# Performance work log

Hardware: AMD Instinct MI355X
Metric: run time of the kernel (lower is better)

## Reference

```python
import jax, jax.numpy as jnp
import numpy as np

MODEL_DIM = 1024
NUM_HEADS = 8
B, L = 16, 2048


def setup_inputs() -> dict:
    key = jax.random.key(0)
    ks = jax.random.split(key, 12)
    s = 1.0 / np.sqrt(MODEL_DIM)
    d = MODEL_DIM
    return {
        "query": jax.random.normal(ks[0], (B, L, d), jnp.float32),
        "key_": jax.random.normal(ks[1], (B, L, d), jnp.float32),
        "value": jax.random.normal(ks[2], (B, L, d), jnp.float32),
        "Wq": jax.random.uniform(ks[3], (d, d), jnp.float32, -s, s),
        "bq": jax.random.uniform(ks[4], (d,), jnp.float32, -s, s),
        "Wk": jax.random.uniform(ks[5], (d, d), jnp.float32, -s, s),
        "bk": jax.random.uniform(ks[6], (d,), jnp.float32, -s, s),
        "Wv": jax.random.uniform(ks[7], (d, d), jnp.float32, -s, s),
        "bv": jax.random.uniform(ks[8], (d,), jnp.float32, -s, s),
        "Wo": jax.random.uniform(ks[9], (d, d), jnp.float32, -s, s),
        "bo": jax.random.uniform(ks[10], (d,), jnp.float32, -s, s),
    }


def reference(query, key_, value, Wq, bq, Wk, bk, Wv, bv, Wo, bo):
    # NOTE: the original module does NOT split heads; attention is over the
    # full model_dim per batch row. num_heads only enters via the scale.
    residual = query
    q = jnp.einsum("bld,de->ble", query, Wq) + bq
    k = jnp.einsum("bld,de->ble", key_, Wk) + bk
    v = jnp.einsum("bld,de->ble", value, Wv) + bv
    scale = (MODEL_DIM // NUM_HEADS) ** (-0.5)
    attn = jnp.einsum("bqd,bkd->bqk", q, k) * scale  # [B, L, L]
    attn = jax.nn.softmax(attn, axis=-1)
    ctx = jnp.einsum("bqk,bkd->bqd", attn, v)
    out = jnp.einsum("bld,de->ble", ctx, Wo) + bo  # dropout=0.0 -> identity
    return residual + out
```

## Files before the change

### kernel.cpp

```cpp
#include <hip/hip_runtime.h>
#include <cstdint>

#define B_ 16
#define L_ 2048
#define D_ 1024
#define BLROWS (B_ * L_)
#define QK_SCALE 0.08838834764831845f

typedef unsigned short u16;
typedef __attribute__((ext_vector_type(8))) __bf16 bf16x8;
typedef __attribute__((ext_vector_type(4))) float f32x4;
typedef __attribute__((ext_vector_type(4))) unsigned int u32x4;
typedef __attribute__((ext_vector_type(4))) u16 u16x4;

__device__ __forceinline__ u16 f2bf(float f) {
  unsigned u = __builtin_bit_cast(unsigned, f);
  u += 0x7fffu + ((u >> 16) & 1u);
  return (u16)(u >> 16);
}
__device__ __forceinline__ float bf2f(unsigned hu) {
  return __builtin_bit_cast(float, hu << 16);
}

__device__ __forceinline__ void gll16(const void* g, void* l) {
  auto gp = reinterpret_cast<const __attribute__((address_space(1))) unsigned int*>(
      reinterpret_cast<uintptr_t>(g));
  auto lp = reinterpret_cast<__attribute__((address_space(3))) unsigned int*>(
      reinterpret_cast<uintptr_t>(l));
  __builtin_amdgcn_global_load_lds(gp, lp, 16, 0, 0);
}

typedef __attribute__((ext_vector_type(4))) float fv4;
__global__ void convert_bf16(const fv4* __restrict__ in, u16x4* __restrict__ out, int n4) {
  int i = blockIdx.x * blockDim.x + threadIdx.x;
  const int stride = gridDim.x * blockDim.x;
  for (; i < n4; i += stride) {
    fv4 v = in[i];
    u16x4 o;
    o.x = f2bf(v.x); o.y = f2bf(v.y); o.z = f2bf(v.z); o.w = f2bf(v.w);
    out[i] = o;
  }
}

__global__ void transpose_convert_1k(const float* __restrict__ W, u16* __restrict__ WT) {
  __shared__ float tile[32][33];
  const int bx = blockIdx.x * 32;
  const int by = blockIdx.y * 32;
  const int tx = threadIdx.x & 31;
  const int ty = threadIdx.x >> 5;
#pragma unroll
  for (int j = 0; j < 4; ++j) {
    const int r = ty + j * 8;
    tile[r][tx] = W[(size_t)(by + r) * 1024 + bx + tx];
  }
  __syncthreads();
#pragma unroll
  for (int j = 0; j < 4; ++j) {
    const int r = ty + j * 8;
    WT[(size_t)(bx + r) * 1024 + by + tx] = f2bf(tile[tx][r]);
  }
}

__global__ void softmax_rows(u16* __restrict__ S) {
  const size_t row = blockIdx.x;
  u32x4* p = (u32x4*)(S + row * 2048);
  const int t = threadIdx.x;
  u32x4 v = p[t];
  unsigned vv[4] = {v.x, v.y, v.z, v.w};
  float x[8];
#pragma unroll
  for (int i = 0; i < 4; ++i) {
    x[2 * i]     = bf2f(vv[i] & 0xffffu);
    x[2 * i + 1] = bf2f(vv[i] >> 16);
  }
  float m = x[0];
#pragma unroll
  for (int i = 1; i < 8; ++i) m = fmaxf(m, x[i]);
#pragma unroll
  for (int off = 32; off > 0; off >>= 1) m = fmaxf(m, __shfl_xor(m, off));
  __shared__ float red[4];
  const int w = t >> 6, l = t & 63;
  if (l == 0) red[w] = m;
  __syncthreads();
  m = fmaxf(fmaxf(red[0], red[1]), fmaxf(red[2], red[3]));
  float e[8], s = 0.f;
#pragma unroll
  for (int i = 0; i < 8; ++i) { e[i] = __expf(x[i] - m); s += e[i]; }
#pragma unroll
  for (int off = 32; off > 0; off >>= 1) s += __shfl_xor(s, off);
  __syncthreads();
  if (l == 0) red[w] = s;
  __syncthreads();
  s = red[0] + red[1] + red[2] + red[3];
  const float inv = 1.0f / s;
  unsigned oo[4];
#pragma unroll
  for (int i = 0; i < 4; ++i) {
    oo[i] = (unsigned)f2bf(e[2 * i] * inv) | ((unsigned)f2bf(e[2 * i + 1] * inv) << 16);
  }
  u32x4 o; o.x = oo[0]; o.y = oo[1]; o.z = oo[2]; o.w = oo[3];
  p[t] = o;
}


#define MFMA16(QM, QN, BF)                                                    \
  _Pragma("unroll") for (int mf = 0; mf < 4; ++mf)                            \
  _Pragma("unroll") for (int nf = 0; nf < 2; ++nf)                            \
  _Pragma("unroll") for (int kk = 0; kk < 2; ++kk)                            \
      acc[(QM)*4 + mf][(QN)*2 + nf] = __builtin_amdgcn_mfma_f32_16x16x32_bf16( \
          af[mf][kk], BF[nf][kk], acc[(QM)*4 + mf][(QN)*2 + nf], 0, 0, 0);

template <int OUT_BF16, int BIAS_MODE, int RESID>
__global__ __launch_bounds__(512) void gemm8(
    const u16* __restrict__ A, const u16* __restrict__ Bm, void* __restrict__ Cv,
    const float* __restrict__ bias, const float* __restrict__ resid,
    int N, int K, float scale, long long sA, long long sB, long long sC,
    int gm, int gn) {
  __shared__ alignas(16) u16 lds[2][4][128 * 64];

  const int nwg = gridDim.x;
  const int wg = blockIdx.x;
  const int q = nwg >> 3, rr = nwg & 7;
  const int xcd = wg & 7, idx = wg >> 3;
  const int wgid = (xcd < rr ? xcd * (q + 1) : rr * (q + 1) + (xcd - rr) * q) + idx;
  const int z = wgid / (gm * gn);
  const int rem = wgid - z * gm * gn;
  const int my = rem / gn;
  const int nx = rem - my * gn;
  const int m0 = my * 256, n0 = nx * 256;

  A  += (long long)z * sA;
  Bm += (long long)z * sB;

  const int t = threadIdx.x;
  const int w = t >> 6;
  const int l = t & 63;
  const int wm = w >> 2;
  const int wn = w & 3;
  const int lr = l & 15;
  const int lk = l >> 4;

  const int r  = t >> 3;
  const int sl = (t & 7) ^ (r & 7);
  const u16* pa00 = A  + (long long)(m0 +   0 + r) * K + sl * 8;
  const u16* pa01 = A  + (long long)(m0 +  64 + r) * K + sl * 8;
  const u16* pa10 = A  + (long long)(m0 + 128 + r) * K + sl * 8;
  const u16* pa11 = A  + (long long)(m0 + 192 + r) * K + sl * 8;
  const u16* pb00 = Bm + (long long)(n0 +   0 + r) * K + sl * 8;
  const u16* pb01 = Bm + (long long)(n0 +  64 + r) * K + sl * 8;
  const u16* pb10 = Bm + (long long)(n0 + 128 + r) * K + sl * 8;
  const u16* pb11 = Bm + (long long)(n0 + 192 + r) * K + sl * 8;
  const int wo = w * 512;

#define STAGE_TILE_A(LB, KT)                         \
  gll16(pa00 + (KT)*64, (LB) + 0 * 8192 +        wo); \
  gll16(pa01 + (KT)*64, (LB) + 0 * 8192 + 4096 + wo); \
  gll16(pa10 + (KT)*64, (LB) + 1 * 8192 +        wo); \
  gll16(pa11 + (KT)*64, (LB) + 1 * 8192 + 4096 + wo);
#define STAGE_TILE_B(LB, KT)                         \
  gll16(pb00 + (KT)*64, (LB) + 2 * 8192 +        wo); \
  gll16(pb01 + (KT)*64, (LB) + 2 * 8192 + 4096 + wo); \
  gll16(pb10 + (KT)*64, (LB) + 3 * 8192 +        wo); \
  gll16(pb11 + (KT)*64, (LB) + 3 * 8192 + 4096 + wo);

  f32x4 acc[8][4];
#pragma unroll
  for (int i = 0; i < 8; ++i)
#pragma unroll
    for (int j = 0; j < 4; ++j) acc[i][j] = f32x4{0.f, 0.f, 0.f, 0.f};

  const int cs0 = ((0 + lk) ^ (lr & 7)) * 8;
  const int cs1 = ((4 + lk) ^ (lr & 7)) * 8;
  const u16* LA = &lds[0][wm][0];
  const u16* LB_ = &lds[0][2 + (wn >> 1)][0];
  const int brow = (wn & 1) * 64 + lr;

  {
    u16* Lb = &lds[0][0][0];
    STAGE_TILE_A(Lb, 0)
    STAGE_TILE_B(Lb, 0)
  }
  asm volatile("s_waitcnt vmcnt(0)" ::: "memory");
  __builtin_amdgcn_s_barrier();
  __builtin_amdgcn_sched_barrier(0);

  const int NT = K >> 6;
  for (int kt = 0; kt < NT; ++kt) {
    const int br = kt & 1, bs = br ^ 1;
    const bool pf = (kt + 1 < NT);
    const u16* Ra = LA + br * 32768;
    const u16* Rb = LB_ + br * 32768;
    u16* Lb = &lds[bs][0][0];

    bf16x8 af[4][2], bf0[2][2], bf1[2][2];

    if (pf) { STAGE_TILE_A(Lb, kt + 1) }
#pragma unroll
    for (int mf = 0; mf < 4; ++mf) {
      const int row = mf * 16 + lr;
      af[mf][0] = __builtin_bit_cast(bf16x8, *(const u32x4*)&Ra[row * 64 + cs0]);
      af[mf][1] = __builtin_bit_cast(bf16x8, *(const u32x4*)&Ra[row * 64 + cs1]);
    }
#pragma unroll
    for (int nf = 0; nf < 2; ++nf) {
      const int row = brow + nf * 16;
      bf0[nf][0] = __builtin_bit_cast(bf16x8, *(const u32x4*)&Rb[row * 64 + cs0]);
      bf0[nf][1] = __builtin_bit_cast(bf16x8, *(const u32x4*)&Rb[row * 64 + cs1]);
    }
    __builtin_amdgcn_s_barrier();
    __builtin_amdgcn_s_setprio(1);
    MFMA16(0, 0, bf0)
    __builtin_amdgcn_s_setprio(0);
    __builtin_amdgcn_s_barrier();

    if (pf) { STAGE_TILE_B(Lb, kt + 1) }
#pragma unroll
    for (int nf = 0; nf < 2; ++nf) {
      const int row = brow + 32 + nf * 16;
      bf1[nf][0] = __builtin_bit_cast(bf16x8, *(const u32x4*)&Rb[row * 64 + cs0]);
      bf1[nf][1] = __builtin_bit_cast(bf16x8, *(const u32x4*)&Rb[row * 64 + cs1]);
    }
    __builtin_amdgcn_s_barrier();
    __builtin_amdgcn_s_setprio(1);
    MFMA16(0, 1, bf1)
    __builtin_amdgcn_s_setprio(0);
    __builtin_amdgcn_s_barrier();

#pragma unroll
    for (int mf = 0; mf < 4; ++mf) {
      const int row = 64 + mf * 16 + lr;
      af[mf][0] = __builtin_bit_cast(bf16x8, *(const u32x4*)&Ra[row * 64 + cs0]);
      af[mf][1] = __builtin_bit_cast(bf16x8, *(const u32x4*)&Ra[row * 64 + cs1]);
    }
    __builtin_amdgcn_s_barrier();
    __builtin_amdgcn_s_setprio(1);
    MFMA16(1, 1, bf1)
    __builtin_amdgcn_s_setprio(0);
    __builtin_amdgcn_s_barrier();

    __builtin_amdgcn_s_setprio(1);
    MFMA16(1, 0, bf0)
    __builtin_amdgcn_s_setprio(0);

    if (pf) { asm volatile("s_waitcnt vmcnt(0)" ::: "memory"); }
    __builtin_amdgcn_s_barrier();
    __builtin_amdgcn_sched_barrier(0);
  }

  const int crow0 = m0 + wm * 128;
  const int ccol0 = n0 + wn * 64;
#pragma unroll
  for (int mi = 0; mi < 8; ++mi) {
#pragma unroll
    for (int i = 0; i < 4; ++i) {
      const int grow = crow0 + (mi >> 2) * 64 + (mi & 3) * 16 + lk * 4 + i;
#pragma unroll
      for (int nj = 0; nj < 4; ++nj) {
        const int gcol = ccol0 + (nj >> 1) * 32 + (nj & 1) * 16 + lr;
        float v = acc[mi][nj][i] * scale;
        if (BIAS_MODE == 1) v += bias[gcol];
        if (BIAS_MODE == 2) v += bias[grow];
        if (RESID) v += resid[(long long)grow * N + gcol];
        const long long cidx = (long long)z * sC + (long long)grow * N + gcol;
        if (OUT_BF16) ((u16*)Cv)[cidx] = f2bf(v);
        else          ((float*)Cv)[cidx] = v;
      }
    }
  }
}

extern "C" void kernel_launch(void* const* d_in, const int* in_sizes, int n_in,
                              void* d_out, int out_size, void* d_ws, size_t ws_size,
                              hipStream_t stream) {
  const float* query = (const float*)d_in[0];
  const float* key_  = (const float*)d_in[1];
  const float* value = (const float*)d_in[2];
  const float* Wq = (const float*)d_in[3];
  const float* bq = (const float*)d_in[4];
  const float* Wk = (const float*)d_in[5];
  const float* bk = (const float*)d_in[6];
  const float* Wv = (const float*)d_in[7];
  const float* bv = (const float*)d_in[8];
  const float* Wo = (const float*)d_in[9];
  const float* bo = (const float*)d_in[10];
  float* out = (float*)d_out;

  char* ws = (char*)d_ws;
  u16* xq  = (u16*)(ws + 0);
  u16* xk  = (u16*)(ws + 67108864);
  u16* xv  = (u16*)(ws + 134217728);
  u16* wqt = (u16*)(ws + 201326592);
  u16* wkt = (u16*)(ws + 203423744);
  u16* wvt = (u16*)(ws + 205520896);
  u16* wot = (u16*)(ws + 207618048);
  u16* qb  = (u16*)(ws + 209715200);
  u16* kb  = (u16*)(ws + 276824064);
  u16* vt  = (u16*)(ws + 343932928);
  u16* sp  = (u16*)(ws + 0);
  u16* ctx = (u16*)(ws + 134217728);

  const dim3 blk(256);
  const dim3 blk8(512);
  const int n4 = BLROWS * D_ / 4;

  convert_bf16<<<2048, blk, 0, stream>>>((const fv4*)query, (u16x4*)xq, n4);
  convert_bf16<<<2048, blk, 0, stream>>>((const fv4*)key_,  (u16x4*)xk, n4);
  convert_bf16<<<2048, blk, 0, stream>>>((const fv4*)value, (u16x4*)xv, n4);
  transpose_convert_1k<<<dim3(32, 32), blk, 0, stream>>>(Wq, wqt);
  transpose_convert_1k<<<dim3(32, 32), blk, 0, stream>>>(Wk, wkt);
  transpose_convert_1k<<<dim3(32, 32), blk, 0, stream>>>(Wv, wvt);
  transpose_convert_1k<<<dim3(32, 32), blk, 0, stream>>>(Wo, wot);

  gemm8<1, 1, 0><<<dim3(512), blk8, 0, stream>>>(
      xq, wqt, qb, bq, nullptr, D_, D_, 1.0f, 0, 0, 0, 128, 4);
  gemm8<1, 1, 0><<<dim3(512), blk8, 0, stream>>>(
      xk, wkt, kb, bk, nullptr, D_, D_, 1.0f, 0, 0, 0, 128, 4);
  gemm8<1, 2, 0><<<dim3(512), blk8, 0, stream>>>(
      wvt, xv, vt, bv, nullptr, L_, D_, 1.0f,
      0, (long long)L_ * D_, (long long)D_ * L_, 4, 8);
  gemm8<1, 0, 0><<<dim3(1024), blk8, 0, stream>>>(
      qb, kb, sp, nullptr, nullptr, L_, D_, QK_SCALE,
      (long long)L_ * D_, (long long)L_ * D_, (long long)L_ * L_, 8, 8);
  softmax_rows<<<BLROWS, blk, 0, stream>>>(sp);
  gemm8<1, 0, 0><<<dim3(512), blk8, 0, stream>>>(
      sp, vt, ctx, nullptr, nullptr, D_, L_, 1.0f,
      (long long)L_ * L_, (long long)D_ * L_, (long long)L_ * D_, 8, 4);
  gemm8<0, 1, 1><<<dim3(512), blk8, 0, stream>>>(
      ctx, wot, out, bo, query, D_, D_, 1.0f, 0, 0, 0, 128, 4);

  (void)in_sizes; (void)n_in; (void)out_size; (void)ws_size;
}
```

Before: 1.070 ms.

## Restructure GEMM mainloop to 4-stage K=32 LDS pipeline with prefetch depth three

Replaces the double-buffered K=64 tile loop with a four-buffer ring of K=32 slices, keeping three slices of global-to-LDS loads in flight by using partial vmcnt waits instead of draining all loads each iteration. The LDS layout and XOR swizzle change to 32-element rows, and each wave's output fragments are remapped to contiguous 16-row/16-column blocks. The aim is to hide global memory latency behind MFMA work. In exchange, each iteration does half the math between barriers, so barrier overhead per unit of work roughly doubles. The epilogue index mapping changes to match the new fragment layout.

```diff
diff --git a/kernel.cpp b/kernel.cpp
--- a/kernel.cpp
+++ b/kernel.cpp
@@ -103,20 +103,13 @@
 }
 
 
-#define MFMA16(QM, QN, BF)                                                    \
-  _Pragma("unroll") for (int mf = 0; mf < 4; ++mf)                            \
-  _Pragma("unroll") for (int nf = 0; nf < 2; ++nf)                            \
-  _Pragma("unroll") for (int kk = 0; kk < 2; ++kk)                            \
-      acc[(QM)*4 + mf][(QN)*2 + nf] = __builtin_amdgcn_mfma_f32_16x16x32_bf16( \
-          af[mf][kk], BF[nf][kk], acc[(QM)*4 + mf][(QN)*2 + nf], 0, 0, 0);
-
 template <int OUT_BF16, int BIAS_MODE, int RESID>
 __global__ __launch_bounds__(512) void gemm8(
     const u16* __restrict__ A, const u16* __restrict__ Bm, void* __restrict__ Cv,
     const float* __restrict__ bias, const float* __restrict__ resid,
     int N, int K, float scale, long long sA, long long sB, long long sC,
     int gm, int gn) {
-  __shared__ alignas(16) u16 lds[2][4][128 * 64];
+  __shared__ alignas(16) u16 lds[4][16384];
 
   const int nwg = gridDim.x;
   const int wg = blockIdx.x;
@@ -140,28 +133,23 @@
   const int lr = l & 15;
   const int lk = l >> 4;
 
-  const int r  = t >> 3;
-  const int sl = (t & 7) ^ (r & 7);
-  const u16* pa00 = A  + (long long)(m0 +   0 + r) * K + sl * 8;
-  const u16* pa01 = A  + (long long)(m0 +  64 + r) * K + sl * 8;
-  const u16* pa10 = A  + (long long)(m0 + 128 + r) * K + sl * 8;
-  const u16* pa11 = A  + (long long)(m0 + 192 + r) * K + sl * 8;
-  const u16* pb00 = Bm + (long long)(n0 +   0 + r) * K + sl * 8;
-  const u16* pb01 = Bm + (long long)(n0 +  64 + r) * K + sl * 8;
-  const u16* pb10 = Bm + (long long)(n0 + 128 + r) * K + sl * 8;
-  const u16* pb11 = Bm + (long long)(n0 + 192 + r) * K + sl * 8;
-  const int wo = w * 512;
-
-#define STAGE_TILE_A(LB, KT)                         \
-  gll16(pa00 + (KT)*64, (LB) + 0 * 8192 +        wo); \
-  gll16(pa01 + (KT)*64, (LB) + 0 * 8192 + 4096 + wo); \
-  gll16(pa10 + (KT)*64, (LB) + 1 * 8192 +        wo); \
-  gll16(pa11 + (KT)*64, (LB) + 1 * 8192 + 4096 + wo);
-#define STAGE_TILE_B(LB, KT)                         \
-  gll16(pb00 + (KT)*64, (LB) + 2 * 8192 +        wo); \
-  gll16(pb01 + (KT)*64, (LB) + 2 * 8192 + 4096 + wo); \
-  gll16(pb10 + (KT)*64, (LB) + 3 * 8192 +        wo); \
-  gll16(pb11 + (KT)*64, (LB) + 3 * 8192 + 4096 + wo);
+  const int r0 = w * 32 + (l >> 2);
+  const int ksrc = ((l & 3) ^ ((l >> 2) & 3)) * 8;
+  const u16* pA0 = A  + (long long)(m0 + r0) * K + ksrc;
+  const u16* pA1 = pA0 + 16LL * K;
+  const u16* pB0 = Bm + (long long)(n0 + r0) * K + ksrc;
+  const u16* pB1 = pB0 + 16LL * K;
+  const int dA = w * 1024;
+
+#define STAGEU(U, BUFP)                           \
+  gll16(pA0 + (U) * 32, (BUFP) + dA);             \
+  gll16(pA1 + (U) * 32, (BUFP) + dA + 512);       \
+  gll16(pB0 + (U) * 32, (BUFP) + 8192 + dA);      \
+  gll16(pB1 + (U) * 32, (BUFP) + 8192 + dA + 512);
+
+  const int sw8 = (lk ^ (lr & 3)) * 8;
+  const int axo = (wm * 128 + lr) * 32 + sw8;
+  const int bxo = 8192 + (wn * 64 + lr) * 32 + sw8;
 
   f32x4 acc[8][4];
 #pragma unroll
@@ -169,80 +157,56 @@
 #pragma unroll
     for (int j = 0; j < 4; ++j) acc[i][j] = f32x4{0.f, 0.f, 0.f, 0.f};
 
-  const int cs0 = ((0 + lk) ^ (lr & 7)) * 8;
-  const int cs1 = ((4 + lk) ^ (lr & 7)) * 8;
-  const u16* LA = &lds[0][wm][0];
-  const u16* LB_ = &lds[0][2 + (wn >> 1)][0];
-  const int brow = (wn & 1) * 64 + lr;
-
-  {
-    u16* Lb = &lds[0][0][0];
-    STAGE_TILE_A(Lb, 0)
-    STAGE_TILE_B(Lb, 0)
-  }
-  asm volatile("s_waitcnt vmcnt(0)" ::: "memory");
+  u16* Lb = &lds[0][0];
+
+  STAGEU(0, Lb)
+  STAGEU(1, Lb + 16384)
+  STAGEU(2, Lb + 32768)
+  asm volatile("s_waitcnt vmcnt(8)" ::: "memory");
   __builtin_amdgcn_s_barrier();
   __builtin_amdgcn_sched_barrier(0);
 
-  const int NT = K >> 6;
-  for (int kt = 0; kt < NT; ++kt) {
-    const int br = kt & 1, bs = br ^ 1;
-    const bool pf = (kt + 1 < NT);
-    const u16* Ra = LA + br * 32768;
-    const u16* Rb = LB_ + br * 32768;
-    u16* Lb = &lds[bs][0][0];
-
-    bf16x8 af[4][2], bf0[2][2], bf1[2][2];
-
-    if (pf) { STAGE_TILE_A(Lb, kt + 1) }
-#pragma unroll
-    for (int mf = 0; mf < 4; ++mf) {
-      const int row = mf * 16 + lr;
-      af[mf][0] = __builtin_bit_cast(bf16x8, *(const u32x4*)&Ra[row * 64 + cs0]);
-      af[mf][1] = __builtin_bit_cast(bf16x8, *(const u32x4*)&Ra[row * 64 + cs1]);
-    }
-#pragma unroll
-    for (int nf = 0; nf < 2; ++nf) {
-      const int row = brow + nf * 16;
-      bf0[nf][0] = __builtin_bit_cast(bf16x8, *(const u32x4*)&Rb[row * 64 + cs0]);
-      bf0[nf][1] = __builtin_bit_cast(bf16x8, *(const u32x4*)&Rb[row * 64 + cs1]);
-    }
+  const int NT = K >> 5;
+  for (int u = 0; u < NT; ++u) {
+    const u16* cb = Lb + (u & 3) * 16384;
+    u16* sb = Lb + ((u + 3) & 3) * 16384;
+
+    bf16x8 af[4], bf[4], ag[4];
+
+    if (u + 3 < NT) { STAGEU(u + 3, sb) }
+#pragma unroll
+    for (int mf = 0; mf < 4; ++mf)
+      af[mf] = __builtin_bit_cast(bf16x8, *(const u32x4*)&cb[axo + mf * 512]);
+#pragma unroll
+    for (int nf = 0; nf < 4; ++nf)
+      bf[nf] = __builtin_bit_cast(bf16x8, *(const u32x4*)&cb[bxo + nf * 512]);
     __builtin_amdgcn_s_barrier();
     __builtin_amdgcn_s_setprio(1);
-    MFMA16(0, 0, bf0)
+#pragma unroll
+    for (int mf = 0; mf < 4; ++mf)
+#pragma unroll
+      for (int nf = 0; nf < 4; ++nf)
+        acc[mf][nf] =
+            __builtin_amdgcn_mfma_f32_16x16x32_bf16(af[mf], bf[nf], acc[mf][nf], 0, 0, 0);
     __builtin_amdgcn_s_setprio(0);
     __builtin_amdgcn_s_barrier();
 
-    if (pf) { STAGE_TILE_B(Lb, kt + 1) }
-#pragma unroll
-    for (int nf = 0; nf < 2; ++nf) {
-      const int row = brow + 32 + nf * 16;
-      bf1[nf][0] = __builtin_bit_cast(bf16x8, *(const u32x4*)&Rb[row * 64 + cs0]);
-      bf1[nf][1] = __builtin_bit_cast(bf16x8, *(const u32x4*)&Rb[row * 64 + cs1]);
-    }
+#pragma unroll
+    for (int mf = 0; mf < 4; ++mf)
+      ag[mf] = __builtin_bit_cast(bf16x8, *(const u32x4*)&cb[axo + (mf + 4) * 512]);
     __builtin_amdgcn_s_barrier();
     __builtin_amdgcn_s_setprio(1);
-    MFMA16(0, 1, bf1)
+#pragma unroll
+    for (int mf = 0; mf < 4; ++mf)
+#pragma unroll
+      for (int nf = 0; nf < 4; ++nf)
+        acc[mf + 4][nf] =
+            __builtin_amdgcn_mfma_f32_16x16x32_bf16(ag[mf], bf[nf], acc[mf + 4][nf], 0, 0, 0);
     __builtin_amdgcn_s_setprio(0);
-    __builtin_amdgcn_s_barrier();
-
-#pragma unroll
-    for (int mf = 0; mf < 4; ++mf) {
-      const int row = 64 + mf * 16 + lr;
-      af[mf][0] = __builtin_bit_cast(bf16x8, *(const u32x4*)&Ra[row * 64 + cs0]);
-      af[mf][1] = __builtin_bit_cast(bf16x8, *(const u32x4*)&Ra[row * 64 + cs1]);
-    }
-    __builtin_amdgcn_s_barrier();
-    __builtin_amdgcn_s_setprio(1);
-    MFMA16(1, 1, bf1)
-    __builtin_amdgcn_s_setprio(0);
-    __builtin_amdgcn_s_barrier();
-
-    __builtin_amdgcn_s_setprio(1);
-    MFMA16(1, 0, bf0)
-    __builtin_amdgcn_s_setprio(0);
-
-    if (pf) { asm volatile("s_waitcnt vmcnt(0)" ::: "memory"); }
+
+    if (u + 3 < NT)      { asm volatile("s_waitcnt vmcnt(8)" ::: "memory"); }
+    else if (u + 2 < NT) { asm volatile("s_waitcnt vmcnt(4)" ::: "memory"); }
+    else if (u + 1 < NT) { asm volatile("s_waitcnt vmcnt(0)" ::: "memory"); }
     __builtin_amdgcn_s_barrier();
     __builtin_amdgcn_sched_barrier(0);
   }
@@ -253,10 +217,10 @@
   for (int mi = 0; mi < 8; ++mi) {
 #pragma unroll
     for (int i = 0; i < 4; ++i) {
-      const int grow = crow0 + (mi >> 2) * 64 + (mi & 3) * 16 + lk * 4 + i;
+      const int grow = crow0 + mi * 16 + lk * 4 + i;
 #pragma unroll
       for (int nj = 0; nj < 4; ++nj) {
-        const int gcol = ccol0 + (nj >> 1) * 32 + (nj & 1) * 16 + lr;
+        const int gcol = ccol0 + nj * 16 + lr;
         float v = acc[mi][nj][i] * scale;
         if (BIAS_MODE == 1) v += bias[gcol];
         if (BIAS_MODE == 2) v += bias[grow];
```

After: 1.141 ms. +6.6%, slower.
